# Kernel optimization log

Hardware: AMD Instinct MI355X
Metric: run time of the kernel (lower is better)

The kernel has to match this reference:

```python
import jax, jax.numpy as jnp
import numpy as np

T, D, E, K = 16384, 2048, 128, 8

def setup_inputs() -> dict:
    key = jax.random.key(0)
    k1, k2 = jax.random.split(key)
    hidden_states = jax.random.normal(k1, (T, D), dtype=jnp.float32)
    weight = jax.random.normal(k2, (E, D), dtype=jnp.float32) * 0.02
    return {"hidden_states": hidden_states, "weight": weight}

def reference(hidden_states, weight):
    # (T, D) @ (D, E) -> (T, E) router logits
    x = hidden_states.reshape(-1, weight.shape[1])
    logits = jnp.einsum('td,ed->te', x, weight)
    # softmax in float32 over experts
    router_logits = jax.nn.softmax(logits.astype(jnp.float32), axis=-1)
    # top-k selection + renormalization so selected weights sum to 1
    router_weights, router_indices = jax.lax.top_k(router_logits, K)
    router_weights = router_weights / jnp.sum(router_weights, axis=-1, keepdims=True)
    return (router_logits, router_weights, router_indices)
```

## Files before the change

kernel.cpp:

```cpp
#include <hip/hip_runtime.h>
#include <math.h>


constexpr int T = 16384;
constexpr int D = 2048;
constexpr int E = 128;
constexpr int K = 8;

constexpr int BM  = 32;
constexpr int NS  = 5;
constexpr int NB2 = D / 128;

typedef int i32x4 __attribute__((ext_vector_type(4)));

#define MFI8(A, B, C) C = __builtin_amdgcn_mfma_i32_16x16x64_i8(A, B, C, 0, 0, 0)

#define LGKM_BARRIER() do {                                   \
    asm volatile("s_waitcnt lgkmcnt(0)" ::: "memory");        \
    __builtin_amdgcn_s_barrier();                             \
} while (0)

__device__ __forceinline__ void slice5(float x, float c, float ic, int out[NS]) {
    float r = x;
#pragma unroll
    for (int s = 0; s < NS; ++s) {
        float q = rintf(r * c);
        out[s] = (int)q;
        r = fmaf(q, -ic, r);
        c *= 128.f;
        ic *= (1.f / 128.f);
    }
}

__global__ __launch_bounds__(256)
void w_slice(const float* __restrict__ W, signed char* __restrict__ Ws)
{
    const int e  = blockIdx.x >> 1;
    const int k0 = ((blockIdx.x & 1) << 10) | (threadIdx.x << 2);
    float4 v = *(const float4*)(W + (size_t)e * D + k0);
    int b0[NS], b1[NS], b2[NS], b3[NS];
    slice5(v.x, 512.f, 1.f / 512.f, b0);
    slice5(v.y, 512.f, 1.f / 512.f, b1);
    slice5(v.z, 512.f, 1.f / 512.f, b2);
    slice5(v.w, 512.f, 1.f / 512.f, b3);
#pragma unroll
    for (int s = 0; s < NS; ++s) {
        unsigned lo = __builtin_amdgcn_perm((unsigned)b1[s], (unsigned)b0[s], 0x00000400u);
        unsigned hi = __builtin_amdgcn_perm((unsigned)b3[s], (unsigned)b2[s], 0x00000400u);
        unsigned pk = __builtin_amdgcn_perm(hi, lo, 0x05040100u);
        *(int*)(Ws + (size_t)s * E * D + (size_t)e * D + k0) = (int)pk;
    }
}

__global__ __launch_bounds__(512, 4)
void router_fused(const float* __restrict__ X,
                  const signed char* __restrict__ Ws,
                  float* __restrict__ out)
{
    __shared__ __align__(16) signed char As[2][2][NS][2][4][16][16];
    __shared__ double Ld[BM][E];

    const int tid = threadIdx.x;
    const long t0 = (long)blockIdx.x * BM;

    const int ar = tid >> 4;
    const int ac = (tid & 15) << 2;
    const float* Xp = X + (t0 + ar) * (long)D + ac;

    const int l  = tid & 63;
    const int wv = tid >> 6;
    const int er = l & 15;
    const int kg = l >> 4;

    const size_t wbase = (size_t)(wv * 16 + er) * D + (size_t)kg * 16;
    const signed char* Wq0 = Ws + 0UL * E * D + wbase;
    const signed char* Wq1 = Ws + 1UL * E * D + wbase;
    const signed char* Wq2 = Ws + 2UL * E * D + wbase;
    const signed char* Wq3 = Ws + 3UL * E * D + wbase;
    const signed char* Wq4 = Ws + 4UL * E * D + wbase;

    const int loff = l * 16;

    i32x4 e0 = {}, e1 = {}, e2 = {}, e3 = {}, e4 = {};
    i32x4 f0 = {}, f1 = {}, f2 = {}, f3 = {}, f4 = {};

    auto stage = [&](const float4& v, int buf, int chn) {
        int q0[NS], q1[NS], q2[NS], q3[NS];
        slice5(v.x, 16.f, 1.f / 16.f, q0);
        slice5(v.y, 16.f, 1.f / 16.f, q1);
        slice5(v.z, 16.f, 1.f / 16.f, q2);
        slice5(v.w, 16.f, 1.f / 16.f, q3);
        int* dst = (int*)&As[buf][chn][0][ar >> 4][ac >> 4][ar & 15][ac & 15];
#pragma unroll
        for (int s = 0; s < NS; ++s) {
            unsigned lo = __builtin_amdgcn_perm((unsigned)q1[s], (unsigned)q0[s], 0x00000400u);
            unsigned hi = __builtin_amdgcn_perm((unsigned)q3[s], (unsigned)q2[s], 0x00000400u);
            unsigned pk = __builtin_amdgcn_perm(hi, lo, 0x05040100u);
            dst[s * 512] = (int)pk;
        }
    };

    auto chunkMM = [&](const signed char* ap,
                       const i32x4& b0, const i32x4& b1, const i32x4& b2,
                       const i32x4& b3, const i32x4& b4) {
        i32x4 at0, at1;
        __builtin_amdgcn_s_setprio(1);
        at0 = *(const i32x4*)(ap);           at1 = *(const i32x4*)(ap + 1024);
        MFI8(at0, b0, e0); MFI8(at0, b1, e1); MFI8(at0, b2, e2); MFI8(at0, b3, e3); MFI8(at0, b4, e4);
        MFI8(at1, b0, f0); MFI8(at1, b1, f1); MFI8(at1, b2, f2); MFI8(at1, b3, f3); MFI8(at1, b4, f4);
        at0 = *(const i32x4*)(ap + 2048);    at1 = *(const i32x4*)(ap + 3072);
        MFI8(at0, b0, e1); MFI8(at0, b1, e2); MFI8(at0, b2, e3); MFI8(at0, b3, e4);
        MFI8(at1, b0, f1); MFI8(at1, b1, f2); MFI8(at1, b2, f3); MFI8(at1, b3, f4);
        at0 = *(const i32x4*)(ap + 4096);    at1 = *(const i32x4*)(ap + 5120);
        MFI8(at0, b0, e2); MFI8(at0, b1, e3); MFI8(at0, b2, e4);
        MFI8(at1, b0, f2); MFI8(at1, b1, f3); MFI8(at1, b2, f4);
        at0 = *(const i32x4*)(ap + 6144);    at1 = *(const i32x4*)(ap + 7168);
        MFI8(at0, b0, e3); MFI8(at0, b1, e4);
        MFI8(at1, b0, f3); MFI8(at1, b1, f4);
        at0 = *(const i32x4*)(ap + 8192);    at1 = *(const i32x4*)(ap + 9216);
        MFI8(at0, b0, e4);
        MFI8(at1, b0, f4);
        __builtin_amdgcn_s_setprio(0);
    };

    float4 xv0, xv1;
    {
        float4 x0 = *(const float4*)(Xp);
        float4 x1 = *(const float4*)(Xp + 64);
        stage(x0, 0, 0);
        stage(x1, 0, 1);
        xv0 = *(const float4*)(Xp + 128);
        xv1 = *(const float4*)(Xp + 192);
        LGKM_BARRIER();
    }

    for (int p = 0; p < NB2; ++p) {
        const int cur = p & 1;
        const long kb = (long)p * 128;

        i32x4 b00 = *(const i32x4*)(Wq0 + kb);
        i32x4 b01 = *(const i32x4*)(Wq1 + kb);
        i32x4 b02 = *(const i32x4*)(Wq2 + kb);
        i32x4 b03 = *(const i32x4*)(Wq3 + kb);
        i32x4 b04 = *(const i32x4*)(Wq4 + kb);
        i32x4 b10 = *(const i32x4*)(Wq0 + kb + 64);
        i32x4 b11 = *(const i32x4*)(Wq1 + kb + 64);
        i32x4 b12 = *(const i32x4*)(Wq2 + kb + 64);
        i32x4 b13 = *(const i32x4*)(Wq3 + kb + 64);
        i32x4 b14 = *(const i32x4*)(Wq4 + kb + 64);

        const signed char* ap =
            (const signed char*)&As[cur][0][0][0][0][0][0] + loff;

        chunkMM(ap, b00, b01, b02, b03, b04);

        if (p < NB2 - 1) {
            stage(xv0, cur ^ 1, 0);
            stage(xv1, cur ^ 1, 1);
        }

        chunkMM(ap + 10240, b10, b11, b12, b13, b14);

        if (p < NB2 - 2) {
            const long kn = (long)(p + 2) * 128;
            xv0 = *(const float4*)(Xp + kn);
            xv1 = *(const float4*)(Xp + kn + 64);
        }

        LGKM_BARRIER();
    }

#pragma unroll
    for (int r = 0; r < 4; ++r) {
        const int row = kg * 4 + r;
        const int col = wv * 16 + er;
        Ld[row][col]      = (double)e0[r] * 0x1p-13 + (double)e1[r] * 0x1p-20
                          + (double)e2[r] * 0x1p-27 + (double)e3[r] * 0x1p-34
                          + (double)e4[r] * 0x1p-41;
        Ld[row + 16][col] = (double)f0[r] * 0x1p-13 + (double)f1[r] * 0x1p-20
                          + (double)f2[r] * 0x1p-27 + (double)f3[r] * 0x1p-34
                          + (double)f4[r] * 0x1p-41;
    }
    __syncthreads();

    float* outL  = out;
    float* outWt = out + (long)T * E;
    float* outId = outWt + (long)T * K;
    const int tx = tid & 15;
    const int tt = tid >> 4;
    const long t = t0 + tt;

    double acc[8];
#pragma unroll
    for (int j = 0; j < 8; ++j) acc[j] = Ld[tt][(tx << 3) + j];

    double m = acc[0];
#pragma unroll
    for (int j = 1; j < 8; ++j) m = fmax(m, acc[j]);
#pragma unroll
    for (int mask = 1; mask <= 8; mask <<= 1)
        m = fmax(m, __shfl_xor(m, mask, 64));

    float e[8]; float s = 0.f;
#pragma unroll
    for (int j = 0; j < 8; ++j) { e[j] = __expf((float)(acc[j] - m)); s += e[j]; }
#pragma unroll
    for (int mask = 1; mask <= 8; mask <<= 1)
        s += __shfl_xor(s, mask, 64);
    const float inv = 1.f / s;

    float4 st0 = {e[0] * inv, e[1] * inv, e[2] * inv, e[3] * inv};
    float4 st1 = {e[4] * inv, e[5] * inv, e[6] * inv, e[7] * inv};
    *(float4*)&outL[t * E + (tx << 3)]     = st0;
    *(float4*)&outL[t * E + (tx << 3) + 4] = st1;

    double v[8];
#pragma unroll
    for (int j = 0; j < 8; ++j) v[j] = acc[j];

    float pk[K]; int ik[K]; float tsum = 0.f;
#pragma unroll
    for (int r = 0; r < K; ++r) {
        double bv = -1.0e300; int bi = 0x7fffffff;
#pragma unroll
        for (int j = 0; j < 8; ++j) {
            const int idx = (tx << 3) + j;
            const bool better = (v[j] > bv) || (v[j] == bv && idx < bi);
            bv = better ? v[j] : bv;
            bi = better ? idx : bi;
        }
#pragma unroll
        for (int mask = 1; mask <= 8; mask <<= 1) {
            const double ov = __shfl_xor(bv, mask, 64);
            const int    oi = __shfl_xor(bi, mask, 64);
            const bool better = (ov > bv) || (ov == bv && oi < bi);
            bv = better ? ov : bv;
            bi = better ? oi : bi;
        }
        const float pw = __expf((float)(bv - m)) * inv;
        pk[r] = pw; ik[r] = bi; tsum += pw;
        const bool own  = ((bi >> 3) == tx);
        const int  slot = bi & 7;
#pragma unroll
        for (int j = 0; j < 8; ++j)
            v[j] = (own && j == slot) ? -1.0e300 : v[j];
    }

    if (tx == 0) {
        const float rinv = 1.f / tsum;
#pragma unroll
        for (int r = 0; r < K; ++r) {
            outWt[t * K + r] = pk[r] * rinv;
            outId[t * K + r] = (float)ik[r];
        }
    }
}

extern "C" void kernel_launch(void* const* d_in, const int* in_sizes, int n_in,
                              void* d_out, int out_size, void* d_ws, size_t ws_size,
                              hipStream_t stream)
{
    const float* X = (const float*)d_in[0];
    const float* W = (const float*)d_in[1];
    float* out = (float*)d_out;
    signed char* Ws = (signed char*)d_ws;

    w_slice<<<dim3(E * 2), dim3(256), 0, stream>>>(W, Ws);
    router_fused<<<dim3(T / BM), dim3(512), 0, stream>>>(X, Ws, out);
}
```

Before: 252.9 us.

## Split block into two warp groups alternating MFMA compute and operand staging

Block size grows to 1024 threads, split into two groups of 8 waves. In each 64-wide K chunk one group runs the int8 MFMA chunk while the other loads X and W and quantizes the next chunk into a 4-deep LDS ring. This is meant to hide the global-load and slicing latency behind tensor-core work. Each group keeps its own partial accumulators, and these are summed through LDS before the softmax/top-k epilogue, which only the first 512 threads run. The costs are one barrier per chunk instead of per two chunks, a split-K reduction, and fewer resident blocks per CU given the 1024-thread launch bound.

Result: slower. 302.6 us (+19.6%).

```diff
diff --git a/kernel.cpp b/kernel.cpp
--- a/kernel.cpp
+++ b/kernel.cpp
@@ -7,9 +7,9 @@
 constexpr int E = 128;
 constexpr int K = 8;
 
-constexpr int BM  = 32;
-constexpr int NS  = 5;
-constexpr int NB2 = D / 128;
+constexpr int BM = 32;
+constexpr int NS = 5;
+constexpr int NC = D / 64;
 
 typedef int i32x4 __attribute__((ext_vector_type(4)));
 
@@ -52,27 +52,29 @@
     }
 }
 
-__global__ __launch_bounds__(512, 4)
+__global__ __launch_bounds__(1024, 4)
 void router_fused(const float* __restrict__ X,
                   const signed char* __restrict__ Ws,
                   float* __restrict__ out)
 {
-    __shared__ __align__(16) signed char As[2][2][NS][2][4][16][16];
+    __shared__ __align__(16) signed char As[4][NS][2][4][16][16];
     __shared__ double Ld[BM][E];
 
     const int tid = threadIdx.x;
     const long t0 = (long)blockIdx.x * BM;
 
-    const int ar = tid >> 4;
-    const int ac = (tid & 15) << 2;
-    const float* Xp = X + (t0 + ar) * (long)D + ac;
-
-    const int l  = tid & 63;
-    const int wv = tid >> 6;
-    const int er = l & 15;
-    const int kg = l >> 4;
-
-    const size_t wbase = (size_t)(wv * 16 + er) * D + (size_t)kg * 16;
+    const int l   = tid & 63;
+    const int wv  = tid >> 6;
+    const int grp = wv >> 3;
+    const int er  = l & 15;
+    const int kg  = l >> 4;
+
+    const int s_tid = tid & 511;
+    const int ar    = s_tid >> 4;
+    const int koff  = (s_tid & 15) << 2;
+    const float* Xp = X + (t0 + ar) * (long)D + koff;
+
+    const size_t wbase = (size_t)((wv & 7) * 16 + er) * D + (size_t)kg * 16;
     const signed char* Wq0 = Ws + 0UL * E * D + wbase;
     const signed char* Wq1 = Ws + 1UL * E * D + wbase;
     const signed char* Wq2 = Ws + 2UL * E * D + wbase;
@@ -83,14 +85,15 @@
 
     i32x4 e0 = {}, e1 = {}, e2 = {}, e3 = {}, e4 = {};
     i32x4 f0 = {}, f1 = {}, f2 = {}, f3 = {}, f4 = {};
-
-    auto stage = [&](const float4& v, int buf, int chn) {
+    i32x4 bc0, bc1, bc2, bc3, bc4;
+
+    auto stageChunk = [&](const float4& v, int buf) {
         int q0[NS], q1[NS], q2[NS], q3[NS];
         slice5(v.x, 16.f, 1.f / 16.f, q0);
         slice5(v.y, 16.f, 1.f / 16.f, q1);
         slice5(v.z, 16.f, 1.f / 16.f, q2);
         slice5(v.w, 16.f, 1.f / 16.f, q3);
-        int* dst = (int*)&As[buf][chn][0][ar >> 4][ac >> 4][ar & 15][ac & 15];
+        int* dst = (int*)&As[buf][0][ar >> 4][koff >> 4][ar & 15][koff & 15];
 #pragma unroll
         for (int s = 0; s < NS; ++s) {
             unsigned lo = __builtin_amdgcn_perm((unsigned)q1[s], (unsigned)q0[s], 0x00000400u);
@@ -123,135 +126,140 @@
         __builtin_amdgcn_s_setprio(0);
     };
 
-    float4 xv0, xv1;
     {
-        float4 x0 = *(const float4*)(Xp);
-        float4 x1 = *(const float4*)(Xp + 64);
-        stage(x0, 0, 0);
-        stage(x1, 0, 1);
-        xv0 = *(const float4*)(Xp + 128);
-        xv1 = *(const float4*)(Xp + 192);
+        float4 v = *(const float4*)(Xp + (tid >> 9) * 64);
+        stageChunk(v, tid >> 9);
+    }
+    bc0 = *(const i32x4*)(Wq0 + grp * 64);
+    bc1 = *(const i32x4*)(Wq1 + grp * 64);
+    bc2 = *(const i32x4*)(Wq2 + grp * 64);
+    bc3 = *(const i32x4*)(Wq3 + grp * 64);
+    bc4 = *(const i32x4*)(Wq4 + grp * 64);
+    float4 xv = *(const float4*)(Xp + (3 - grp) * 64);
+    LGKM_BARRIER();
+
+    for (int t = 0; t < NC; ++t) {
+        if (grp == (t & 1)) {
+            const signed char* ap =
+                (const signed char*)&As[t & 3][0][0][0][0][0] + loff;
+            chunkMM(ap, bc0, bc1, bc2, bc3, bc4);
+        } else {
+            float4 xn = xv;
+            if (t + 4 < NC) xn = *(const float4*)(Xp + (t + 4) * 64);
+            if (t + 1 < NC) {
+                const long kc = (long)(t + 1) * 64;
+                bc0 = *(const i32x4*)(Wq0 + kc);
+                bc1 = *(const i32x4*)(Wq1 + kc);
+                bc2 = *(const i32x4*)(Wq2 + kc);
+                bc3 = *(const i32x4*)(Wq3 + kc);
+                bc4 = *(const i32x4*)(Wq4 + kc);
+            }
+            __builtin_amdgcn_sched_barrier(0);
+            if (t + 2 < NC) stageChunk(xv, (t + 2) & 3);
+            xv = xn;
+        }
         LGKM_BARRIER();
     }
 
-    for (int p = 0; p < NB2; ++p) {
-        const int cur = p & 1;
-        const long kb = (long)p * 128;
-
-        i32x4 b00 = *(const i32x4*)(Wq0 + kb);
-        i32x4 b01 = *(const i32x4*)(Wq1 + kb);
-        i32x4 b02 = *(const i32x4*)(Wq2 + kb);
-        i32x4 b03 = *(const i32x4*)(Wq3 + kb);
-        i32x4 b04 = *(const i32x4*)(Wq4 + kb);
-        i32x4 b10 = *(const i32x4*)(Wq0 + kb + 64);
-        i32x4 b11 = *(const i32x4*)(Wq1 + kb + 64);
-        i32x4 b12 = *(const i32x4*)(Wq2 + kb + 64);
-        i32x4 b13 = *(const i32x4*)(Wq3 + kb + 64);
-        i32x4 b14 = *(const i32x4*)(Wq4 + kb + 64);
-
-        const signed char* ap =
-            (const signed char*)&As[cur][0][0][0][0][0][0] + loff;
-
-        chunkMM(ap, b00, b01, b02, b03, b04);
-
-        if (p < NB2 - 1) {
-            stage(xv0, cur ^ 1, 0);
-            stage(xv1, cur ^ 1, 1);
-        }
-
-        chunkMM(ap + 10240, b10, b11, b12, b13, b14);
-
-        if (p < NB2 - 2) {
-            const long kn = (long)(p + 2) * 128;
-            xv0 = *(const float4*)(Xp + kn);
-            xv1 = *(const float4*)(Xp + kn + 64);
-        }
-
-        LGKM_BARRIER();
-    }
-
+    double g0[4], g1[4];
 #pragma unroll
     for (int r = 0; r < 4; ++r) {
-        const int row = kg * 4 + r;
-        const int col = wv * 16 + er;
-        Ld[row][col]      = (double)e0[r] * 0x1p-13 + (double)e1[r] * 0x1p-20
-                          + (double)e2[r] * 0x1p-27 + (double)e3[r] * 0x1p-34
-                          + (double)e4[r] * 0x1p-41;
-        Ld[row + 16][col] = (double)f0[r] * 0x1p-13 + (double)f1[r] * 0x1p-20
-                          + (double)f2[r] * 0x1p-27 + (double)f3[r] * 0x1p-34
-                          + (double)f4[r] * 0x1p-41;
-    }
-    __syncthreads();
-
-    float* outL  = out;
-    float* outWt = out + (long)T * E;
-    float* outId = outWt + (long)T * K;
-    const int tx = tid & 15;
-    const int tt = tid >> 4;
-    const long t = t0 + tt;
-
-    double acc[8];
-#pragma unroll
-    for (int j = 0; j < 8; ++j) acc[j] = Ld[tt][(tx << 3) + j];
-
-    double m = acc[0];
-#pragma unroll
-    for (int j = 1; j < 8; ++j) m = fmax(m, acc[j]);
-#pragma unroll
-    for (int mask = 1; mask <= 8; mask <<= 1)
-        m = fmax(m, __shfl_xor(m, mask, 64));
-
-    float e[8]; float s = 0.f;
-#pragma unroll
-    for (int j = 0; j < 8; ++j) { e[j] = __expf((float)(acc[j] - m)); s += e[j]; }
-#pragma unroll
-    for (int mask = 1; mask <= 8; mask <<= 1)
-        s += __shfl_xor(s, mask, 64);
-    const float inv = 1.f / s;
-
-    float4 st0 = {e[0] * inv, e[1] * inv, e[2] * inv, e[3] * inv};
-    float4 st1 = {e[4] * inv, e[5] * inv, e[6] * inv, e[7] * inv};
-    *(float4*)&outL[t * E + (tx << 3)]     = st0;
-    *(float4*)&outL[t * E + (tx << 3) + 4] = st1;
-
-    double v[8];
-#pragma unroll
-    for (int j = 0; j < 8; ++j) v[j] = acc[j];
-
-    float pk[K]; int ik[K]; float tsum = 0.f;
-#pragma unroll
-    for (int r = 0; r < K; ++r) {
-        double bv = -1.0e300; int bi = 0x7fffffff;
-#pragma unroll
-        for (int j = 0; j < 8; ++j) {
-            const int idx = (tx << 3) + j;
-            const bool better = (v[j] > bv) || (v[j] == bv && idx < bi);
-            bv = better ? v[j] : bv;
-            bi = better ? idx : bi;
-        }
-#pragma unroll
-        for (int mask = 1; mask <= 8; mask <<= 1) {
-            const double ov = __shfl_xor(bv, mask, 64);
-            const int    oi = __shfl_xor(bi, mask, 64);
-            const bool better = (ov > bv) || (ov == bv && oi < bi);
-            bv = better ? ov : bv;
-            bi = better ? oi : bi;
-        }
-        const float pw = __expf((float)(bv - m)) * inv;
-        pk[r] = pw; ik[r] = bi; tsum += pw;
-        const bool own  = ((bi >> 3) == tx);
-        const int  slot = bi & 7;
-#pragma unroll
-        for (int j = 0; j < 8; ++j)
-            v[j] = (own && j == slot) ? -1.0e300 : v[j];
-    }
-
-    if (tx == 0) {
-        const float rinv = 1.f / tsum;
+        g0[r] = (double)e0[r] * 0x1p-13 + (double)e1[r] * 0x1p-20
+              + (double)e2[r] * 0x1p-27 + (double)e3[r] * 0x1p-34
+              + (double)e4[r] * 0x1p-41;
+        g1[r] = (double)f0[r] * 0x1p-13 + (double)f1[r] * 0x1p-20
+              + (double)f2[r] * 0x1p-27 + (double)f3[r] * 0x1p-34
+              + (double)f4[r] * 0x1p-41;
+    }
+    const int col = (wv & 7) * 16 + er;
+    if (grp == 0) {
+#pragma unroll
+        for (int r = 0; r < 4; ++r) {
+            Ld[kg * 4 + r][col]      = g0[r];
+            Ld[kg * 4 + r + 16][col] = g1[r];
+        }
+    }
+    LGKM_BARRIER();
+    if (grp == 1) {
+#pragma unroll
+        for (int r = 0; r < 4; ++r) {
+            Ld[kg * 4 + r][col]      += g0[r];
+            Ld[kg * 4 + r + 16][col] += g1[r];
+        }
+    }
+    LGKM_BARRIER();
+
+    if (tid < 512) {
+        float* outL  = out;
+        float* outWt = out + (long)T * E;
+        float* outId = outWt + (long)T * K;
+        const int tx = tid & 15;
+        const int tt = tid >> 4;
+        const long t = t0 + tt;
+
+        double acc[8];
+#pragma unroll
+        for (int j = 0; j < 8; ++j) acc[j] = Ld[tt][(tx << 3) + j];
+
+        double m = acc[0];
+#pragma unroll
+        for (int j = 1; j < 8; ++j) m = fmax(m, acc[j]);
+#pragma unroll
+        for (int mask = 1; mask <= 8; mask <<= 1)
+            m = fmax(m, __shfl_xor(m, mask, 64));
+
+        float e[8]; float s = 0.f;
+#pragma unroll
+        for (int j = 0; j < 8; ++j) { e[j] = __expf((float)(acc[j] - m)); s += e[j]; }
+#pragma unroll
+        for (int mask = 1; mask <= 8; mask <<= 1)
+            s += __shfl_xor(s, mask, 64);
+        const float inv = 1.f / s;
+
+        float4 st0 = {e[0] * inv, e[1] * inv, e[2] * inv, e[3] * inv};
+        float4 st1 = {e[4] * inv, e[5] * inv, e[6] * inv, e[7] * inv};
+        *(float4*)&outL[t * E + (tx << 3)]     = st0;
+        *(float4*)&outL[t * E + (tx << 3) + 4] = st1;
+
+        double v[8];
+#pragma unroll
+        for (int j = 0; j < 8; ++j) v[j] = acc[j];
+
+        float pk[K]; int ik[K]; float tsum = 0.f;
 #pragma unroll
         for (int r = 0; r < K; ++r) {
-            outWt[t * K + r] = pk[r] * rinv;
-            outId[t * K + r] = (float)ik[r];
+            double bv = -1.0e300; int bi = 0x7fffffff;
+#pragma unroll
+            for (int j = 0; j < 8; ++j) {
+                const int idx = (tx << 3) + j;
+                const bool better = (v[j] > bv) || (v[j] == bv && idx < bi);
+                bv = better ? v[j] : bv;
+                bi = better ? idx : bi;
+            }
+#pragma unroll
+            for (int mask = 1; mask <= 8; mask <<= 1) {
+                const double ov = __shfl_xor(bv, mask, 64);
+                const int    oi = __shfl_xor(bi, mask, 64);
+                const bool better = (ov > bv) || (ov == bv && oi < bi);
+                bv = better ? ov : bv;
+                bi = better ? oi : bi;
+            }
+            const float pw = __expf((float)(bv - m)) * inv;
+            pk[r] = pw; ik[r] = bi; tsum += pw;
+            const bool own  = ((bi >> 3) == tx);
+            const int  slot = bi & 7;
+#pragma unroll
+            for (int j = 0; j < 8; ++j)
+                v[j] = (own && j == slot) ? -1.0e300 : v[j];
+        }
+
+        if (tx == 0) {
+            const float rinv = 1.f / tsum;
+#pragma unroll
+            for (int r = 0; r < K; ++r) {
+                outWt[t * K + r] = pk[r] * rinv;
+                outId[t * K + r] = (float)ik[r];
+            }
         }
     }
 }
@@ -266,5 +274,5 @@
     signed char* Ws = (signed char*)d_ws;
 
     w_slice<<<dim3(E * 2), dim3(256), 0, stream>>>(W, Ws);
-    router_fused<<<dim3(T / BM), dim3(512), 0, stream>>>(X, Ws, out);
-}
+    router_fused<<<dim3(T / BM), dim3(1024), 0, stream>>>(X, Ws, out);
+}
```
